# Performance work log

Hardware: AMD Instinct MI355X
Metric: run time of the kernel (lower is better)

Reference implementation:

```python
import jax, jax.numpy as jnp
import numpy as np

N_NODES = 100000
N_EDGES = 1600000
NFEAT = 128
NCLASS = 40


def setup_inputs() -> dict:
    key = jax.random.key(0)
    k1, k2, k3 = jax.random.split(key, 3)
    x = jax.random.normal(k1, (N_NODES, NFEAT), dtype=jnp.float32)
    edge_index = jax.random.randint(k2, (2, N_EDGES), 0, N_NODES, dtype=jnp.int64)
    W = jax.random.normal(k3, (NFEAT, NCLASS), dtype=jnp.float32) * (1.0 / np.sqrt(NFEAT))
    b = jnp.zeros((NCLASS,), dtype=jnp.float32)
    return {"x": x, "edge_index": edge_index, "W": W, "b": b, "k": 3}


def reference(x, edge_index, W, b, k):
    N = x.shape[0]
    # gcn_norm with add_self_loops=True (PyG SGConv default)
    loop = jnp.arange(N, dtype=edge_index.dtype)
    row = jnp.concatenate([edge_index[0], loop])  # source nodes (x_j)
    col = jnp.concatenate([edge_index[1], loop])  # target nodes (aggregation index)
    deg = jax.ops.segment_sum(jnp.ones_like(col, dtype=x.dtype), col, num_segments=N)
    dis = jnp.where(deg > 0, jax.lax.rsqrt(deg), 0.0)  # deg^{-1/2}, inf -> 0
    norm = (dis[row] * dis[col])[:, None]  # [E+N, 1]
    # k hops of sparse propagation: out[col] += norm * x[row]
    for _ in range(k):
        x = jax.ops.segment_sum(norm * x[row], col, num_segments=N)
    # final linear projection
    return x @ W + b
```

## Files before the change

### kernel.cpp

```cpp
#include <hip/hip_runtime.h>

#define N_NODES 100000
#define N_EDGES 1600000
#define NFEAT 128
#define NCLASS 40
#define SCAN_BLK 98


__global__ void cnt_zero(int* __restrict__ cnt) {
    int i = blockIdx.x * blockDim.x + threadIdx.x;
    if (i < N_NODES) cnt[i] = 0;
}

__global__ void cnt_count(const int* __restrict__ col, int* __restrict__ cnt) {
    int e = blockIdx.x * blockDim.x + threadIdx.x;
    if (e < N_EDGES) atomicAdd(&cnt[col[e]], 1);
}

__global__ void dis_from_cnt(const int* __restrict__ cnt, float* __restrict__ dis) {
    int i = blockIdx.x * blockDim.x + threadIdx.x;
    if (i < N_NODES) dis[i] = rsqrtf((float)cnt[i] + 1.0f);
}


__global__ void scan_partial(const int* __restrict__ cnt, int* __restrict__ bsum) {
    __shared__ int red[256];
    int blk = blockIdx.x, tid = threadIdx.x;
    int base = blk * 1024 + tid * 4;
    int s = 0;
    if (base + 3 < N_NODES) {
        int4 v = *reinterpret_cast<const int4*>(cnt + base);
        s = v.x + v.y + v.z + v.w;
    } else {
        for (int i = 0; i < 4; ++i) if (base + i < N_NODES) s += cnt[base + i];
    }
    red[tid] = s;
    __syncthreads();
    for (int o = 128; o > 0; o >>= 1) {
        if (tid < o) red[tid] += red[tid + o];
        __syncthreads();
    }
    if (tid == 0) bsum[blk] = red[0];
}

__global__ void scan_base(int* __restrict__ bsum, int* __restrict__ rowptr) {
    __shared__ int s[128];
    int tid = threadIdx.x;
    s[tid] = (tid < SCAN_BLK) ? bsum[tid] : 0;
    __syncthreads();
    for (int o = 1; o < 128; o <<= 1) {
        int v = s[tid];
        int a = (tid >= o) ? s[tid - o] : 0;
        __syncthreads();
        s[tid] = v + a;
        __syncthreads();
    }
    if (tid < SCAN_BLK) bsum[tid] = (tid == 0) ? 0 : s[tid - 1];
    if (tid == 0) rowptr[N_NODES] = s[SCAN_BLK - 1];
}

__global__ void scan_write(const int* __restrict__ cnt, const int* __restrict__ bsum,
                           int* __restrict__ rowptr, int* __restrict__ cursor) {
    __shared__ int psum[256];
    int blk = blockIdx.x, tid = threadIdx.x;
    int base = blk * 1024 + tid * 4;
    int c0 = 0, c1 = 0, c2 = 0, c3 = 0;
    if (base + 3 < N_NODES) {
        int4 v = *reinterpret_cast<const int4*>(cnt + base);
        c0 = v.x; c1 = v.y; c2 = v.z; c3 = v.w;
    } else {
        if (base < N_NODES)     c0 = cnt[base];
        if (base + 1 < N_NODES) c1 = cnt[base + 1];
        if (base + 2 < N_NODES) c2 = cnt[base + 2];
        if (base + 3 < N_NODES) c3 = cnt[base + 3];
    }
    int s = c0 + c1 + c2 + c3;
    psum[tid] = s;
    __syncthreads();
    for (int o = 1; o < 256; o <<= 1) {
        int v = psum[tid];
        int a = (tid >= o) ? psum[tid - o] : 0;
        __syncthreads();
        psum[tid] = v + a;
        __syncthreads();
    }
    int ex = psum[tid] - s + bsum[blk];
    if (base + 3 < N_NODES) {
        int4 rp = make_int4(ex, ex + c0, ex + c0 + c1, ex + c0 + c1 + c2);
        *reinterpret_cast<int4*>(rowptr + base) = rp;
        *reinterpret_cast<int4*>(cursor + base) = rp;
    } else {
        int r = ex;
        if (base < N_NODES)     { rowptr[base] = r;     cursor[base] = r;     r += c0; }
        if (base + 1 < N_NODES) { rowptr[base + 1] = r; cursor[base + 1] = r; r += c1; }
        if (base + 2 < N_NODES) { rowptr[base + 2] = r; cursor[base + 2] = r; r += c2; }
        if (base + 3 < N_NODES) { rowptr[base + 3] = r; cursor[base + 3] = r; }
    }
}


__global__ void scatter_csr(const int* __restrict__ row, const int* __restrict__ col,
                            const float* __restrict__ dis, int* __restrict__ cursor,
                            int2* __restrict__ csr) {
    int e = blockIdx.x * blockDim.x + threadIdx.x;
    if (e >= N_EDGES) return;
    int r = row[e];
    int c = col[e];
    int slot = atomicAdd(&cursor[c], 1);
    csr[slot] = make_int2(r, __float_as_int(dis[r] * dis[c]));
}


__global__ void gemm_xw(const float* __restrict__ x, const float* __restrict__ W,
                        float* __restrict__ z) {
    int n = blockIdx.x * blockDim.x + threadIdx.x;
    if (n >= N_NODES) return;
    const float4* xr = reinterpret_cast<const float4*>(x + (size_t)n * NFEAT);
    float acc[NCLASS];
#pragma unroll
    for (int c = 0; c < NCLASS; ++c) acc[c] = 0.0f;
    for (int fb = 0; fb < NFEAT / 4; ++fb) {
        float4 xv = xr[fb];
#pragma unroll
        for (int j = 0; j < 4; ++j) {
            float xs = (&xv.x)[j];
            const float* wrow = W + (fb * 4 + j) * NCLASS;
#pragma unroll
            for (int c = 0; c < NCLASS; ++c) acc[c] += xs * wrow[c];
        }
    }
    float4* zr = reinterpret_cast<float4*>(z + (size_t)n * NCLASS);
#pragma unroll
    for (int cb = 0; cb < NCLASS / 4; ++cb)
        zr[cb] = make_float4(acc[cb * 4], acc[cb * 4 + 1], acc[cb * 4 + 2], acc[cb * 4 + 3]);
}


__global__ void hop_pull(const int* __restrict__ rowptr, const int2* __restrict__ csr,
                         const float* __restrict__ dis, const float* __restrict__ zin,
                         const float* __restrict__ b, float* __restrict__ zout) {
    int wid = (blockIdx.x * blockDim.x + threadIdx.x) >> 6;
    int lane = threadIdx.x & 63;
    if (wid >= N_NODES) return;
    int beg = rowptr[wid];
    int end = rowptr[wid + 1];
    float d = dis[wid];
    float acc = 0.0f;
    if (lane < NCLASS) {
        acc = d * d * zin[wid * NCLASS + lane];
        if (b != nullptr) acc += b[lane];
    }
    int k = beg;
    int n4 = beg + ((end - beg) & ~3);
    for (; k < n4; k += 4) {
        int2 p0 = csr[k], p1 = csr[k + 1], p2 = csr[k + 2], p3 = csr[k + 3];
        if (lane < NCLASS) {
            float g0 = zin[p0.x * NCLASS + lane];
            float g1 = zin[p1.x * NCLASS + lane];
            float g2 = zin[p2.x * NCLASS + lane];
            float g3 = zin[p3.x * NCLASS + lane];
            acc += __int_as_float(p0.y) * g0 + __int_as_float(p1.y) * g1
                 + __int_as_float(p2.y) * g2 + __int_as_float(p3.y) * g3;
        }
    }
    for (; k < end; ++k) {
        int2 p = csr[k];
        if (lane < NCLASS) acc += __int_as_float(p.y) * zin[p.x * NCLASS + lane];
    }
    if (lane < NCLASS) zout[wid * NCLASS + lane] = acc;
}


extern "C" void kernel_launch(void* const* d_in, const int* in_sizes, int n_in,
                              void* d_out, int out_size, void* d_ws, size_t ws_size,
                              hipStream_t stream) {
    const float* x = (const float*)d_in[0];
    const int* ei = (const int*)d_in[1];
    const float* W = (const float*)d_in[2];
    const float* b = (const float*)d_in[3];

    const int* row = ei;
    const int* col = ei + N_EDGES;

    char* ws = (char*)d_ws;
    size_t off = 0;
    auto alloc = [&](size_t bytes) { void* p = ws + off; off += (bytes + 255) & ~(size_t)255; return p; };
    int*   cnt    = (int*)  alloc((size_t)N_NODES * 4);
    float* dis    = (float*)alloc((size_t)N_NODES * 4);
    int*   rowptr = (int*)  alloc((size_t)(N_NODES + 1) * 4);
    int*   cursor = (int*)  alloc((size_t)N_NODES * 4);
    int*   bsum   = (int*)  alloc(128 * 4);
    int2*  csr    = (int2*) alloc((size_t)N_EDGES * 8);
    float* buf0   = (float*)alloc((size_t)N_NODES * NCLASS * 4);
    float* outf   = (float*)d_out;

    const int B = 256;
    cnt_zero<<<(N_NODES + B - 1) / B, B, 0, stream>>>(cnt);
    cnt_count<<<(N_EDGES + B - 1) / B, B, 0, stream>>>(col, cnt);
    dis_from_cnt<<<(N_NODES + B - 1) / B, B, 0, stream>>>(cnt, dis);
    scan_partial<<<SCAN_BLK, 256, 0, stream>>>(cnt, bsum);
    scan_base<<<1, 128, 0, stream>>>(bsum, rowptr);
    scan_write<<<SCAN_BLK, 256, 0, stream>>>(cnt, bsum, rowptr, cursor);
    scatter_csr<<<(N_EDGES + B - 1) / B, B, 0, stream>>>(row, col, dis, cursor, csr);

    gemm_xw<<<(N_NODES + B - 1) / B, B, 0, stream>>>(x, W, buf0);

    int grid_hop = (int)(((size_t)N_NODES * 64 + B - 1) / B);
    hop_pull<<<grid_hop, B, 0, stream>>>(rowptr, csr, dis, buf0, nullptr, outf);
    hop_pull<<<grid_hop, B, 0, stream>>>(rowptr, csr, dis, outf, nullptr, buf0);
    hop_pull<<<grid_hop, B, 0, stream>>>(rowptr, csr, dis, buf0, b, outf);
}
```

Baseline: 486.8 us.

## Factor symmetric degree normalization out of edges into per-node scaling

Rewrites the propagation as D^-1/2 A D^-1/2 applied by pre-scaling the features with dis after the GEMM, summing neighbours unweighted, and scaling by d*d between hops (and by d plus the bias on the final hop). This shrinks the CSR entries from int2 (index plus weight) to a plain int index, halving edge-array traffic in the scatter and in every hop, and removes the per-edge multiply. The dis computation is folded into scan_write, which drops one kernel launch. Floating-point summation order and scaling differ slightly from the reference.

```diff
diff --git a/kernel.cpp b/kernel.cpp
--- a/kernel.cpp
+++ b/kernel.cpp
@@ -15,11 +15,6 @@
 __global__ void cnt_count(const int* __restrict__ col, int* __restrict__ cnt) {
     int e = blockIdx.x * blockDim.x + threadIdx.x;
     if (e < N_EDGES) atomicAdd(&cnt[col[e]], 1);
-}
-
-__global__ void dis_from_cnt(const int* __restrict__ cnt, float* __restrict__ dis) {
-    int i = blockIdx.x * blockDim.x + threadIdx.x;
-    if (i < N_NODES) dis[i] = rsqrtf((float)cnt[i] + 1.0f);
 }
 
 
@@ -60,7 +55,8 @@
 }
 
 __global__ void scan_write(const int* __restrict__ cnt, const int* __restrict__ bsum,
-                           int* __restrict__ rowptr, int* __restrict__ cursor) {
+                           int* __restrict__ rowptr, int* __restrict__ cursor,
+                           float* __restrict__ dis) {
     __shared__ int psum[256];
     int blk = blockIdx.x, tid = threadIdx.x;
     int base = blk * 1024 + tid * 4;
@@ -89,30 +85,31 @@
         int4 rp = make_int4(ex, ex + c0, ex + c0 + c1, ex + c0 + c1 + c2);
         *reinterpret_cast<int4*>(rowptr + base) = rp;
         *reinterpret_cast<int4*>(cursor + base) = rp;
+        float4 dv = make_float4(rsqrtf((float)c0 + 1.0f), rsqrtf((float)c1 + 1.0f),
+                                rsqrtf((float)c2 + 1.0f), rsqrtf((float)c3 + 1.0f));
+        *reinterpret_cast<float4*>(dis + base) = dv;
     } else {
         int r = ex;
-        if (base < N_NODES)     { rowptr[base] = r;     cursor[base] = r;     r += c0; }
-        if (base + 1 < N_NODES) { rowptr[base + 1] = r; cursor[base + 1] = r; r += c1; }
-        if (base + 2 < N_NODES) { rowptr[base + 2] = r; cursor[base + 2] = r; r += c2; }
-        if (base + 3 < N_NODES) { rowptr[base + 3] = r; cursor[base + 3] = r; }
+        if (base < N_NODES)     { rowptr[base] = r;     cursor[base] = r;     dis[base] = rsqrtf((float)c0 + 1.0f);     r += c0; }
+        if (base + 1 < N_NODES) { rowptr[base + 1] = r; cursor[base + 1] = r; dis[base + 1] = rsqrtf((float)c1 + 1.0f); r += c1; }
+        if (base + 2 < N_NODES) { rowptr[base + 2] = r; cursor[base + 2] = r; dis[base + 2] = rsqrtf((float)c2 + 1.0f); r += c2; }
+        if (base + 3 < N_NODES) { rowptr[base + 3] = r; cursor[base + 3] = r; dis[base + 3] = rsqrtf((float)c3 + 1.0f); }
     }
 }
 
 
 __global__ void scatter_csr(const int* __restrict__ row, const int* __restrict__ col,
-                            const float* __restrict__ dis, int* __restrict__ cursor,
-                            int2* __restrict__ csr) {
+                            int* __restrict__ cursor, int* __restrict__ csr) {
     int e = blockIdx.x * blockDim.x + threadIdx.x;
     if (e >= N_EDGES) return;
-    int r = row[e];
     int c = col[e];
     int slot = atomicAdd(&cursor[c], 1);
-    csr[slot] = make_int2(r, __float_as_int(dis[r] * dis[c]));
+    csr[slot] = row[e];
 }
 
 
 __global__ void gemm_xw(const float* __restrict__ x, const float* __restrict__ W,
-                        float* __restrict__ z) {
+                        const float* __restrict__ dis, float* __restrict__ z) {
     int n = blockIdx.x * blockDim.x + threadIdx.x;
     if (n >= N_NODES) return;
     const float4* xr = reinterpret_cast<const float4*>(x + (size_t)n * NFEAT);
@@ -129,14 +126,17 @@
             for (int c = 0; c < NCLASS; ++c) acc[c] += xs * wrow[c];
         }
     }
+    float d = dis[n];
     float4* zr = reinterpret_cast<float4*>(z + (size_t)n * NCLASS);
 #pragma unroll
     for (int cb = 0; cb < NCLASS / 4; ++cb)
-        zr[cb] = make_float4(acc[cb * 4], acc[cb * 4 + 1], acc[cb * 4 + 2], acc[cb * 4 + 3]);
-}
-
-
-__global__ void hop_pull(const int* __restrict__ rowptr, const int2* __restrict__ csr,
+        zr[cb] = make_float4(d * acc[cb * 4], d * acc[cb * 4 + 1],
+                             d * acc[cb * 4 + 2], d * acc[cb * 4 + 3]);
+}
+
+
+template <int FINAL>
+__global__ void hop_pull(const int* __restrict__ rowptr, const int* __restrict__ csr,
                          const float* __restrict__ dis, const float* __restrict__ zin,
                          const float* __restrict__ b, float* __restrict__ zout) {
     int wid = (blockIdx.x * blockDim.x + threadIdx.x) >> 6;
@@ -144,30 +144,31 @@
     if (wid >= N_NODES) return;
     int beg = rowptr[wid];
     int end = rowptr[wid + 1];
-    float d = dis[wid];
     float acc = 0.0f;
-    if (lane < NCLASS) {
-        acc = d * d * zin[wid * NCLASS + lane];
-        if (b != nullptr) acc += b[lane];
-    }
+    if (lane < NCLASS) acc = zin[wid * NCLASS + lane];
     int k = beg;
     int n4 = beg + ((end - beg) & ~3);
     for (; k < n4; k += 4) {
-        int2 p0 = csr[k], p1 = csr[k + 1], p2 = csr[k + 2], p3 = csr[k + 3];
+        int p0 = csr[k], p1 = csr[k + 1], p2 = csr[k + 2], p3 = csr[k + 3];
         if (lane < NCLASS) {
-            float g0 = zin[p0.x * NCLASS + lane];
-            float g1 = zin[p1.x * NCLASS + lane];
-            float g2 = zin[p2.x * NCLASS + lane];
-            float g3 = zin[p3.x * NCLASS + lane];
-            acc += __int_as_float(p0.y) * g0 + __int_as_float(p1.y) * g1
-                 + __int_as_float(p2.y) * g2 + __int_as_float(p3.y) * g3;
+            float g0 = zin[p0 * NCLASS + lane];
+            float g1 = zin[p1 * NCLASS + lane];
+            float g2 = zin[p2 * NCLASS + lane];
+            float g3 = zin[p3 * NCLASS + lane];
+            acc += g0 + g1 + g2 + g3;
         }
     }
     for (; k < end; ++k) {
-        int2 p = csr[k];
-        if (lane < NCLASS) acc += __int_as_float(p.y) * zin[p.x * NCLASS + lane];
-    }
-    if (lane < NCLASS) zout[wid * NCLASS + lane] = acc;
+        int p = csr[k];
+        if (lane < NCLASS) acc += zin[p * NCLASS + lane];
+    }
+    if (lane < NCLASS) {
+        float d = dis[wid];
+        float r;
+        if (FINAL) r = d * acc + b[lane];
+        else       r = d * d * acc;
+        zout[wid * NCLASS + lane] = r;
+    }
 }
 
 
@@ -190,23 +191,22 @@
     int*   rowptr = (int*)  alloc((size_t)(N_NODES + 1) * 4);
     int*   cursor = (int*)  alloc((size_t)N_NODES * 4);
     int*   bsum   = (int*)  alloc(128 * 4);
-    int2*  csr    = (int2*) alloc((size_t)N_EDGES * 8);
+    int*   csr    = (int*)  alloc((size_t)N_EDGES * 4);
     float* buf0   = (float*)alloc((size_t)N_NODES * NCLASS * 4);
     float* outf   = (float*)d_out;
 
     const int B = 256;
     cnt_zero<<<(N_NODES + B - 1) / B, B, 0, stream>>>(cnt);
     cnt_count<<<(N_EDGES + B - 1) / B, B, 0, stream>>>(col, cnt);
-    dis_from_cnt<<<(N_NODES + B - 1) / B, B, 0, stream>>>(cnt, dis);
     scan_partial<<<SCAN_BLK, 256, 0, stream>>>(cnt, bsum);
     scan_base<<<1, 128, 0, stream>>>(bsum, rowptr);
-    scan_write<<<SCAN_BLK, 256, 0, stream>>>(cnt, bsum, rowptr, cursor);
-    scatter_csr<<<(N_EDGES + B - 1) / B, B, 0, stream>>>(row, col, dis, cursor, csr);
-
-    gemm_xw<<<(N_NODES + B - 1) / B, B, 0, stream>>>(x, W, buf0);
+    scan_write<<<SCAN_BLK, 256, 0, stream>>>(cnt, bsum, rowptr, cursor, dis);
+    scatter_csr<<<(N_EDGES + B - 1) / B, B, 0, stream>>>(row, col, cursor, csr);
+
+    gemm_xw<<<(N_NODES + B - 1) / B, B, 0, stream>>>(x, W, dis, buf0);
 
     int grid_hop = (int)(((size_t)N_NODES * 64 + B - 1) / B);
-    hop_pull<<<grid_hop, B, 0, stream>>>(rowptr, csr, dis, buf0, nullptr, outf);
-    hop_pull<<<grid_hop, B, 0, stream>>>(rowptr, csr, dis, outf, nullptr, buf0);
-    hop_pull<<<grid_hop, B, 0, stream>>>(rowptr, csr, dis, buf0, b, outf);
-}
+    hop_pull<0><<<grid_hop, B, 0, stream>>>(rowptr, csr, dis, buf0, nullptr, outf);
+    hop_pull<0><<<grid_hop, B, 0, stream>>>(rowptr, csr, dis, outf, nullptr, buf0);
+    hop_pull<1><<<grid_hop, B, 0, stream>>>(rowptr, csr, dis, buf0, b, outf);
+}
```

Measured after the change: 529.0 us. 8.7% more time.
